# Kernel tuning notes

Hardware: AMD Instinct MI355X
Metric: run time of the kernel (lower is better)

Reference implementation:

```python
import jax, jax.numpy as jnp
import numpy as np

N = 50000      # nodes
E = 800000     # directed edges (avg degree 16)
IN, HID, OUT = 256, 128, 16


def setup_inputs() -> dict:
    key = jax.random.key(0)
    ks = jax.random.split(key, 8)
    x = jax.random.normal(ks[0], (N, IN), dtype=jnp.float32)
    edge_index = jax.random.randint(ks[1], (2, E), 0, N)
    W1 = jax.random.normal(ks[2], (IN, HID), dtype=jnp.float32) * (1.0 / np.sqrt(IN))
    b1 = jnp.zeros((HID,), jnp.float32)
    W2 = jax.random.normal(ks[3], (HID, HID), dtype=jnp.float32) * (1.0 / np.sqrt(HID))
    b2 = jnp.zeros((HID,), jnp.float32)
    Wc = jax.random.normal(ks[4], (HID, OUT), dtype=jnp.float32) * (1.0 / np.sqrt(HID))
    bc = jnp.zeros((OUT,), jnp.float32)
    return {"x": x, "W1": W1, "b1": b1, "W2": W2, "b2": b2,
            "Wc": Wc, "bc": bc, "edge_index": edge_index, "conv_time": 30}


def _gcn_norm(edge_index, n, dtype):
    # add self-loops, compute symmetric GCN normalization D^{-1/2}(A+I)D^{-1/2}
    loops = jnp.arange(n)
    src = jnp.concatenate([edge_index[0], loops])
    dst = jnp.concatenate([edge_index[1], loops])
    deg = jax.ops.segment_sum(jnp.ones_like(dst, dtype=dtype), dst, num_segments=n)
    dinv = jnp.where(deg > 0, jax.lax.rsqrt(deg), jnp.zeros_like(deg))
    norm = dinv[src] * dinv[dst]          # [E+N] edge weights
    return src, dst, norm


def _propagate(h, src, dst, norm, n, hops):
    # hops is a static Python int (conv_time)
    for _ in range(hops):
        h = jax.ops.segment_sum(h[src] * norm[:, None], dst, num_segments=n)
    return h


def reference(x, W1, b1, W2, b2, Wc, bc, edge_index, conv_time):
    n = x.shape[0]
    src, dst, norm = _gcn_norm(edge_index, n, x.dtype)
    # conv1: linear only (conv_time = 0)
    h = jax.nn.relu(x @ W1 + b1)
    # dropout is identity in eval mode
    # conv2: linear + conv_time hops of normalized propagation
    h = _propagate(h @ W2 + b2, src, dst, norm, n, int(conv_time))
    h = jax.nn.relu(h)
    # cls: linear + 1 hop
    h = _propagate(h @ Wc + bc, src, dst, norm, n, 1)
    return h
```

## Files before the change

kernel.cpp:

```cpp
#include <hip/hip_runtime.h>
#include <hip/hip_fp16.h>

#define NNODES 50000
#define NEDGES 800000
#define IN_F   256
#define HID_F  128
#define OUT_F  16
#define HOPS   30
#define MPAD   50048

typedef unsigned int u32;
typedef unsigned long long u64;
typedef _Float16 f16;
typedef f16 f16x8 __attribute__((ext_vector_type(8)));
typedef float f32x4 __attribute__((ext_vector_type(4)));
typedef u32 u32x4 __attribute__((ext_vector_type(4)));

union U32H2 { u32 u; __half2 h; };

__device__ inline float2 upk(u32 v) {
    U32H2 t; t.u = v;
    return __half22float2(t.h);
}
__device__ inline u32 pk2(float a, float b) {
    U32H2 t; t.h = __floats2half2_rn(a, b);
    return t.u;
}


__global__ void k_init_deg(int* __restrict__ deg, int n) {
    int i = blockIdx.x * blockDim.x + threadIdx.x;
    if (i < n) deg[i] = 1;
}

__global__ void k_count(const int* __restrict__ dst, int* __restrict__ deg, int e) {
    int i = blockIdx.x * blockDim.x + threadIdx.x;
    if (i < e) atomicAdd(&deg[dst[i]], 1);
}

__global__ void k_dinv(const int* __restrict__ deg, float* __restrict__ dinv, int n) {
    int i = blockIdx.x * blockDim.x + threadIdx.x;
    if (i < n) dinv[i] = rsqrtf((float)deg[i]);
}

__global__ void k_scan1(const int* __restrict__ deg, int* __restrict__ bsums, int n) {
    __shared__ int sh[256];
    int tid = threadIdx.x;
    int i = blockIdx.x * 256 + tid;
    sh[tid] = (i < n) ? deg[i] : 0;
    __syncthreads();
    for (int ofs = 128; ofs > 0; ofs >>= 1) {
        if (tid < ofs) sh[tid] += sh[tid + ofs];
        __syncthreads();
    }
    if (tid == 0) bsums[blockIdx.x] = sh[0];
}

__global__ void k_scan2(int* __restrict__ bsums, int nb, int* __restrict__ rp, int n) {
    if (threadIdx.x == 0 && blockIdx.x == 0) {
        int run = 0;
        for (int b = 0; b < nb; ++b) { int t = bsums[b]; bsums[b] = run; run += t; }
        rp[n] = run;
    }
}

__global__ void k_scan3(const int* __restrict__ deg, const int* __restrict__ bsums,
                        int* __restrict__ rp, int* __restrict__ cursor, int n) {
    __shared__ int sh[256];
    int tid = threadIdx.x;
    int i = blockIdx.x * 256 + tid;
    int v = (i < n) ? deg[i] : 0;
    sh[tid] = v;
    __syncthreads();
    for (int ofs = 1; ofs < 256; ofs <<= 1) {
        int t = 0;
        if (tid >= ofs) t = sh[tid - ofs];
        __syncthreads();
        sh[tid] += t;
        __syncthreads();
    }
    if (i < n) {
        int excl = sh[tid] - v + bsums[blockIdx.x];
        rp[i] = excl;
        cursor[i] = excl;
    }
}

__global__ void k_scatter(const int* __restrict__ src, const int* __restrict__ dst,
                          const float* __restrict__ dinv, int* __restrict__ cursor,
                          int2* __restrict__ ew, int e, int n) {
    int t = blockIdx.x * blockDim.x + threadIdx.x;
    if (t < e) {
        int s = src[t], d = dst[t];
        int pos = atomicAdd(&cursor[d], 1);
        ew[pos] = make_int2(s, __float_as_int(dinv[s] * dinv[d]));
    } else if (t < e + n) {
        int i = t - e;
        int pos = atomicAdd(&cursor[i], 1);
        float di = dinv[i];
        ew[pos] = make_int2(i, __float_as_int(di * di));
    }
}

__global__ void k_sortwave(const int* __restrict__ rp, int2* __restrict__ ew, int n) {
    int node = blockIdx.x * 4 + (threadIdx.x >> 6);
    int lane = threadIdx.x & 63;
    if (node >= n) return;
    int beg = rp[node], end = rp[node + 1];
    int deg = end - beg;
    if (deg > 64) return;
    int2 my = make_int2(0x7fffffff, 0);
    if (lane < deg) my = ew[beg + lane];
    int rank = 0;
    for (int k = 0; k < deg; ++k) {
        int sk = __shfl(my.x, k);
        rank += (sk < my.x) || (sk == my.x && k < lane);
    }
    if (lane < deg) ew[beg + rank] = my;
}

template<int K, int NC>
__global__ void k_cast_wt(const float* __restrict__ W, f16* __restrict__ Wt) {
    int i = blockIdx.x * blockDim.x + threadIdx.x;
    if (i < K * NC) {
        int k = i / NC, c = i % NC;
        Wt[(size_t)c * K + k] = (f16)W[i];
    }
}


template<int K, bool RELU, typename TA>
__global__ __launch_bounds__(256)
void k_gemm_mfma(const TA* __restrict__ A, const f16* __restrict__ Wt,
                 const float* __restrict__ b, f16* __restrict__ C, int M) {
    __shared__ f16 sa[64][K + 8];
    int tid  = threadIdx.x;
    int wid  = tid >> 6;
    int lane = tid & 63;
    int row0 = blockIdx.x * 64;
    int rowW = row0 + wid * 16;
    int rl   = lane & 15;
    int kc   = (lane >> 4) * 8;

    if constexpr (sizeof(TA) == 4) {
        const float4* A4 = reinterpret_cast<const float4*>(A);
        constexpr int C4 = K / 4;
        for (int idx = tid; idx < 64 * C4; idx += 256) {
            int r  = idx / C4;
            int c4 = idx % C4;
            int gr = row0 + r;
            if (gr >= M) gr = M - 1;
            float4 v = A4[(size_t)gr * C4 + c4];
            f16 o[4] = {(f16)v.x, (f16)v.y, (f16)v.z, (f16)v.w};
            *reinterpret_cast<u64*>(&sa[r][c4 * 4]) = *reinterpret_cast<u64*>(o);
        }
    } else {
        const u32x4* A4 = reinterpret_cast<const u32x4*>(A);
        constexpr int C8 = K / 8;
        for (int idx = tid; idx < 64 * C8; idx += 256) {
            int r  = idx / C8;
            int c8 = idx % C8;
            int gr = row0 + r;
            if (gr >= M) gr = M - 1;
            u32x4 v = A4[(size_t)gr * C8 + c8];
            *reinterpret_cast<u32x4*>(&sa[r][c8 * 8]) = v;
        }
    }
    __syncthreads();

    f32x4 acc[8];
#pragma unroll
    for (int n = 0; n < 8; ++n) acc[n] = (f32x4)0.f;

    int lr = wid * 16 + rl;
#pragma unroll
    for (int k0 = 0; k0 < K; k0 += 32) {
        f16x8 aF = *reinterpret_cast<const f16x8*>(&sa[lr][k0 + kc]);
#pragma unroll
        for (int n = 0; n < 8; ++n) {
            f16x8 bF = *reinterpret_cast<const f16x8*>(
                Wt + (size_t)(n * 16 + rl) * K + k0 + kc);
            acc[n] = __builtin_amdgcn_mfma_f32_16x16x32_f16(aF, bF, acc[n], 0, 0, 0);
        }
    }

#pragma unroll
    for (int n = 0; n < 8; ++n) {
        int col = n * 16 + rl;
        float bias = b[col];
#pragma unroll
        for (int j = 0; j < 4; ++j) {
            int row = rowW + 4 * (lane >> 4) + j;
            if (row < M) {
                float s = acc[n][j] + bias;
                if (RELU) s = fmaxf(s, 0.f);
                C[(size_t)row * 128 + col] = (f16)s;
            }
        }
    }
}


template<bool RELU>
__global__ void k_proph(const u32* __restrict__ Hin, u32* __restrict__ Hout,
                        const int* __restrict__ rp, const int2* __restrict__ ew,
                        int n) {
    int grp  = threadIdx.x >> 4;
    int lane = threadIdx.x & 15;
    int node = blockIdx.x * 16 + grp;
    if (node >= n) return;
    int beg = rp[node], end = rp[node + 1];
    const u32x4* H4 = reinterpret_cast<const u32x4*>(Hin);

    float acc[8];
#pragma unroll
    for (int i = 0; i < 8; ++i) acc[i] = 0.f;

    auto body = [&](int e) {
        int2 p   = ew[e];
        float ww = __int_as_float(p.y);
        u32x4 v  = H4[(size_t)p.x * 16 + lane];
#pragma unroll
        for (int q = 0; q < 4; ++q) {
            float2 f = upk(v[q]);
            acc[q * 2 + 0] += ww * f.x;
            acc[q * 2 + 1] += ww * f.y;
        }
    };

    int e = beg;
    for (; e + 1 < end; e += 2) { body(e); body(e + 1); }
    if (e < end) body(e);

    if (RELU) {
#pragma unroll
        for (int i = 0; i < 8; ++i) acc[i] = fmaxf(acc[i], 0.f);
    }
    u32x4 o;
#pragma unroll
    for (int q = 0; q < 4; ++q) o[q] = pk2(acc[q * 2], acc[q * 2 + 1]);
    reinterpret_cast<u32x4*>(Hout)[(size_t)node * 16 + lane] = o;
}


__global__ void k_cls_h(const u32* __restrict__ Ah, const float* __restrict__ Wc,
                        const float* __restrict__ bc, float* __restrict__ G, int M) {
    __shared__ float sa[64][132];
    __shared__ float4 sw4[512];
    int tid  = threadIdx.x;
    int row0 = blockIdx.x * 64;

    for (int idx = tid; idx < 512; idx += 256)
        sw4[idx] = reinterpret_cast<const float4*>(Wc)[idx];

    const uint4* A4 = reinterpret_cast<const uint4*>(Ah);
    for (int idx = tid; idx < 64 * 16; idx += 256) {
        int r = idx >> 4, c = idx & 15;
        int gr = row0 + r;
        uint4 v = (gr < M) ? A4[(size_t)gr * 16 + c]
                           : make_uint4(0u, 0u, 0u, 0u);
        float* dst = &sa[r][c * 8];
        const u32* vv = reinterpret_cast<const u32*>(&v);
#pragma unroll
        for (int q = 0; q < 4; ++q) {
            float2 f = upk(vv[q]);
            dst[q * 2 + 0] = f.x;
            dst[q * 2 + 1] = f.y;
        }
    }
    __syncthreads();

    int tc = tid & 3;
    int tr = tid >> 2;
    float4 acc = make_float4(0.f, 0.f, 0.f, 0.f);
    for (int k4 = 0; k4 < 32; ++k4) {
        float4 a = *reinterpret_cast<const float4*>(&sa[tr][k4 * 4]);
        const float* af = reinterpret_cast<const float*>(&a);
#pragma unroll
        for (int kk = 0; kk < 4; ++kk) {
            float4 wv = sw4[(k4 * 4 + kk) * 4 + tc];
            float av = af[kk];
            acc.x += av * wv.x; acc.y += av * wv.y;
            acc.z += av * wv.z; acc.w += av * wv.w;
        }
    }
    int r = row0 + tr;
    if (r < M) {
        float4 bb = reinterpret_cast<const float4*>(bc)[tc];
        acc.x += bb.x; acc.y += bb.y; acc.z += bb.z; acc.w += bb.w;
        reinterpret_cast<float4*>(G)[(size_t)r * 4 + tc] = acc;
    }
}


__global__ void k_prop16(const float* __restrict__ Gin, float* __restrict__ Out,
                         const int* __restrict__ rp, const int2* __restrict__ ew,
                         int n) {
    int g    = blockIdx.x * 64 + (threadIdx.x >> 2);
    int lane = threadIdx.x & 3;
    if (g >= n) return;
    int beg = rp[g], end = rp[g + 1];
    const float4* G4 = reinterpret_cast<const float4*>(Gin);
    float ax = 0.f, ay = 0.f, az = 0.f, aw = 0.f;
    for (int e = beg; e < end; ++e) {
        int2 p   = ew[e];
        float ww = __int_as_float(p.y);
        float4 hv = G4[(size_t)p.x * 4 + lane];
        ax += ww * hv.x; ay += ww * hv.y; az += ww * hv.z; aw += ww * hv.w;
    }
    reinterpret_cast<float4*>(Out)[(size_t)g * 4 + lane] = make_float4(ax, ay, az, aw);
}


extern "C" void kernel_launch(void* const* d_in, const int* in_sizes, int n_in,
                              void* d_out, int out_size, void* d_ws, size_t ws_size,
                              hipStream_t stream) {
    const float* x  = (const float*)d_in[0];
    const float* W1 = (const float*)d_in[1];
    const float* b1 = (const float*)d_in[2];
    const float* W2 = (const float*)d_in[3];
    const float* b2 = (const float*)d_in[4];
    const float* Wc = (const float*)d_in[5];
    const float* bc = (const float*)d_in[6];
    const int*   ei = (const int*)d_in[7];
    const int* srcp = ei;
    const int* dstp = ei + NEDGES;
    float* out = (float*)d_out;

    char* p = (char*)d_ws;
    auto alloc = [&](size_t bytes) -> char* {
        char* r = p;
        p += (bytes + 255) & ~(size_t)255;
        return r;
    };
    int*   deg    = (int*)  alloc(NNODES * 4);
    float* dinv   = (float*)alloc(NNODES * 4);
    int*   rp     = (int*)  alloc((NNODES + 1) * 4);
    int*   cursor = (int*)  alloc(NNODES * 4);
    int*   bsums  = (int*)  alloc(256 * 4);
    int2*  ew     = (int2*) alloc((size_t)(NEDGES + NNODES) * 8);
    f16*   W1t    = (f16*)  alloc((size_t)HID_F * IN_F * 2);
    f16*   W2t    = (f16*)  alloc((size_t)HID_F * HID_F * 2);
    f16*   H0h    = (f16*)  alloc((size_t)MPAD * HID_F * 2);
    u32*   Hh0    = (u32*)  alloc((size_t)MPAD * HID_F * 2);
    u32*   Hh1    = (u32*)  alloc((size_t)NNODES * HID_F * 2);
    float* G      = (float*)alloc((size_t)NNODES * OUT_F * 4);

    const int T = 256;
    auto nb = [](int n, int t) { return (n + t - 1) / t; };

    k_init_deg<<<nb(NNODES, T), T, 0, stream>>>(deg, NNODES);
    k_count<<<nb(NEDGES, T), T, 0, stream>>>(dstp, deg, NEDGES);
    k_dinv<<<nb(NNODES, T), T, 0, stream>>>(deg, dinv, NNODES);
    int NB = nb(NNODES, 256);
    k_scan1<<<NB, 256, 0, stream>>>(deg, bsums, NNODES);
    k_scan2<<<1, 1, 0, stream>>>(bsums, NB, rp, NNODES);
    k_scan3<<<NB, 256, 0, stream>>>(deg, bsums, rp, cursor, NNODES);
    k_scatter<<<nb(NEDGES + NNODES, T), T, 0, stream>>>(srcp, dstp, dinv, cursor,
                                                        ew, NEDGES, NNODES);
    k_sortwave<<<nb(NNODES, 4), 256, 0, stream>>>(rp, ew, NNODES);

    k_cast_wt<IN_F,  HID_F><<<nb(IN_F * HID_F, T), T, 0, stream>>>(W1, W1t);
    k_cast_wt<HID_F, HID_F><<<nb(HID_F * HID_F, T), T, 0, stream>>>(W2, W2t);

    int GB = MPAD / 64;
    k_gemm_mfma<IN_F,  true,  float><<<GB, 256, 0, stream>>>(x,   W1t, b1, H0h, NNODES);
    k_gemm_mfma<HID_F, false, f16  ><<<GB, 256, 0, stream>>>(H0h, W2t, b2, (f16*)Hh0, NNODES);

    u32* cur = Hh0;
    u32* nxt = Hh1;
    int PB = nb(NNODES, 16);
    for (int i = 0; i < HOPS; ++i) {
        if (i == HOPS - 1)
            k_proph<true ><<<PB, 256, 0, stream>>>(cur, nxt, rp, ew, NNODES);
        else
            k_proph<false><<<PB, 256, 0, stream>>>(cur, nxt, rp, ew, NNODES);
        u32* t = cur; cur = nxt; nxt = t;
    }

    k_cls_h<<<nb(NNODES, 64), 256, 0, stream>>>(cur, Wc, bc, G, NNODES);
    k_prop16<<<nb(NNODES, 64), 256, 0, stream>>>(G, out, rp, ew, NNODES);
}
```

Before: 1.094 ms.

## Bucket nodes by degree for propagation and stage GEMM weights in LDS

Builds a degree histogram and counting-sort permutation so the 30 propagation hops process nodes grouped by similar degree. This is meant to reduce load imbalance between the 16-lane groups within a wavefront. Separately, the MFMA GEMM now loads weight tiles into shared memory in K-chunks instead of reading B fragments directly from global memory. The costs are an extra indirection per node, output writes and rp reads that are no longer coalesced, and more LDS use in the GEMM.

```diff
diff --git a/kernel.cpp b/kernel.cpp
--- a/kernel.cpp
+++ b/kernel.cpp
@@ -119,6 +119,28 @@
     if (lane < deg) ew[beg + rank] = my;
 }
 
+
+__global__ void k_hist(const int* __restrict__ deg, int* __restrict__ hist, int n) {
+    int i = blockIdx.x * blockDim.x + threadIdx.x;
+    if (i < n) atomicAdd(&hist[min(deg[i], 64)], 1);
+}
+
+__global__ void k_histscan(int* __restrict__ hist, int* __restrict__ bincur) {
+    if (threadIdx.x == 0 && blockIdx.x == 0) {
+        int run = 0;
+        for (int b = 0; b <= 64; ++b) { int t = hist[b]; bincur[b] = run; run += t; }
+    }
+}
+
+__global__ void k_permscatter(const int* __restrict__ deg, int* __restrict__ bincur,
+                              int* __restrict__ perm, int n) {
+    int i = blockIdx.x * blockDim.x + threadIdx.x;
+    if (i < n) {
+        int pos = atomicAdd(&bincur[min(deg[i], 64)], 1);
+        perm[pos] = i;
+    }
+}
+
 template<int K, int NC>
 __global__ void k_cast_wt(const float* __restrict__ W, f16* __restrict__ Wt) {
     int i = blockIdx.x * blockDim.x + threadIdx.x;
@@ -133,7 +155,9 @@
 __global__ __launch_bounds__(256)
 void k_gemm_mfma(const TA* __restrict__ A, const f16* __restrict__ Wt,
                  const float* __restrict__ b, f16* __restrict__ C, int M) {
-    __shared__ f16 sa[64][K + 8];
+    constexpr int KC = (K > 128) ? 128 : K;
+    __shared__ f16 sa[64][KC + 8];
+    __shared__ f16 sb[128][KC + 8];
     int tid  = threadIdx.x;
     int wid  = tid >> 6;
     int lane = tid & 63;
@@ -142,45 +166,59 @@
     int rl   = lane & 15;
     int kc   = (lane >> 4) * 8;
 
-    if constexpr (sizeof(TA) == 4) {
-        const float4* A4 = reinterpret_cast<const float4*>(A);
-        constexpr int C4 = K / 4;
-        for (int idx = tid; idx < 64 * C4; idx += 256) {
-            int r  = idx / C4;
-            int c4 = idx % C4;
-            int gr = row0 + r;
-            if (gr >= M) gr = M - 1;
-            float4 v = A4[(size_t)gr * C4 + c4];
-            f16 o[4] = {(f16)v.x, (f16)v.y, (f16)v.z, (f16)v.w};
-            *reinterpret_cast<u64*>(&sa[r][c4 * 4]) = *reinterpret_cast<u64*>(o);
-        }
-    } else {
-        const u32x4* A4 = reinterpret_cast<const u32x4*>(A);
-        constexpr int C8 = K / 8;
-        for (int idx = tid; idx < 64 * C8; idx += 256) {
-            int r  = idx / C8;
-            int c8 = idx % C8;
-            int gr = row0 + r;
-            if (gr >= M) gr = M - 1;
-            u32x4 v = A4[(size_t)gr * C8 + c8];
-            *reinterpret_cast<u32x4*>(&sa[r][c8 * 8]) = v;
-        }
-    }
-    __syncthreads();
-
     f32x4 acc[8];
 #pragma unroll
     for (int n = 0; n < 8; ++n) acc[n] = (f32x4)0.f;
 
     int lr = wid * 16 + rl;
-#pragma unroll
-    for (int k0 = 0; k0 < K; k0 += 32) {
-        f16x8 aF = *reinterpret_cast<const f16x8*>(&sa[lr][k0 + kc]);
-#pragma unroll
-        for (int n = 0; n < 8; ++n) {
-            f16x8 bF = *reinterpret_cast<const f16x8*>(
-                Wt + (size_t)(n * 16 + rl) * K + k0 + kc);
-            acc[n] = __builtin_amdgcn_mfma_f32_16x16x32_f16(aF, bF, acc[n], 0, 0, 0);
+
+    for (int c = 0; c < K / KC; ++c) {
+        int k0 = c * KC;
+        if (c > 0) __syncthreads();
+        if constexpr (sizeof(TA) == 4) {
+            const float4* A4 = reinterpret_cast<const float4*>(A);
+            constexpr int C4 = KC / 4;
+            for (int idx = tid; idx < 64 * C4; idx += 256) {
+                int r  = idx / C4;
+                int c4 = idx % C4;
+                int gr = row0 + r;
+                if (gr >= M) gr = M - 1;
+                float4 v = A4[(size_t)gr * (K / 4) + k0 / 4 + c4];
+                f16 o[4] = {(f16)v.x, (f16)v.y, (f16)v.z, (f16)v.w};
+                *reinterpret_cast<u64*>(&sa[r][c4 * 4]) = *reinterpret_cast<u64*>(o);
+            }
+        } else {
+            const u32x4* A4 = reinterpret_cast<const u32x4*>(A);
+            constexpr int C8 = KC / 8;
+            for (int idx = tid; idx < 64 * C8; idx += 256) {
+                int r  = idx / C8;
+                int c8 = idx % C8;
+                int gr = row0 + r;
+                if (gr >= M) gr = M - 1;
+                u32x4 v = A4[(size_t)gr * (K / 8) + k0 / 8 + c8];
+                *reinterpret_cast<u32x4*>(&sa[r][c8 * 8]) = v;
+            }
+        }
+        {
+            const u32x4* B4 = reinterpret_cast<const u32x4*>(Wt);
+            constexpr int C8 = KC / 8;
+            for (int idx = tid; idx < 128 * C8; idx += 256) {
+                int r  = idx / C8;
+                int c8 = idx % C8;
+                u32x4 v = B4[(size_t)r * (K / 8) + k0 / 8 + c8];
+                *reinterpret_cast<u32x4*>(&sb[r][c8 * 8]) = v;
+            }
+        }
+        __syncthreads();
+
+#pragma unroll
+        for (int kk = 0; kk < KC; kk += 32) {
+            f16x8 aF = *reinterpret_cast<const f16x8*>(&sa[lr][kk + kc]);
+#pragma unroll
+            for (int n = 0; n < 8; ++n) {
+                f16x8 bF = *reinterpret_cast<const f16x8*>(&sb[n * 16 + rl][kk + kc]);
+                acc[n] = __builtin_amdgcn_mfma_f32_16x16x32_f16(aF, bF, acc[n], 0, 0, 0);
+            }
         }
     }
 
@@ -204,11 +242,12 @@
 template<bool RELU>
 __global__ void k_proph(const u32* __restrict__ Hin, u32* __restrict__ Hout,
                         const int* __restrict__ rp, const int2* __restrict__ ew,
-                        int n) {
+                        const int* __restrict__ perm, int n) {
     int grp  = threadIdx.x >> 4;
     int lane = threadIdx.x & 15;
-    int node = blockIdx.x * 16 + grp;
-    if (node >= n) return;
+    int g    = blockIdx.x * 16 + grp;
+    if (g >= n) return;
+    int node = perm[g];
     int beg = rp[node], end = rp[node + 1];
     const u32x4* H4 = reinterpret_cast<const u32x4*>(Hin);
 
@@ -338,6 +377,9 @@
     int*   rp     = (int*)  alloc((NNODES + 1) * 4);
     int*   cursor = (int*)  alloc(NNODES * 4);
     int*   bsums  = (int*)  alloc(256 * 4);
+    int*   hist   = (int*)  alloc(65 * 4);
+    int*   bincur = (int*)  alloc(65 * 4);
+    int*   perm   = (int*)  alloc(NNODES * 4);
     int2*  ew     = (int2*) alloc((size_t)(NEDGES + NNODES) * 8);
     f16*   W1t    = (f16*)  alloc((size_t)HID_F * IN_F * 2);
     f16*   W2t    = (f16*)  alloc((size_t)HID_F * HID_F * 2);
@@ -359,6 +401,10 @@
     k_scatter<<<nb(NEDGES + NNODES, T), T, 0, stream>>>(srcp, dstp, dinv, cursor,
                                                         ew, NEDGES, NNODES);
     k_sortwave<<<nb(NNODES, 4), 256, 0, stream>>>(rp, ew, NNODES);
+    hipMemsetAsync(hist, 0, 65 * 4, stream);
+    k_hist<<<nb(NNODES, T), T, 0, stream>>>(deg, hist, NNODES);
+    k_histscan<<<1, 1, 0, stream>>>(hist, bincur);
+    k_permscatter<<<nb(NNODES, T), T, 0, stream>>>(deg, bincur, perm, NNODES);
 
     k_cast_wt<IN_F,  HID_F><<<nb(IN_F * HID_F, T), T, 0, stream>>>(W1, W1t);
     k_cast_wt<HID_F, HID_F><<<nb(HID_F * HID_F, T), T, 0, stream>>>(W2, W2t);
@@ -372,9 +418,9 @@
     int PB = nb(NNODES, 16);
     for (int i = 0; i < HOPS; ++i) {
         if (i == HOPS - 1)
-            k_proph<true ><<<PB, 256, 0, stream>>>(cur, nxt, rp, ew, NNODES);
+            k_proph<true ><<<PB, 256, 0, stream>>>(cur, nxt, rp, ew, perm, NNODES);
         else
-            k_proph<false><<<PB, 256, 0, stream>>>(cur, nxt, rp, ew, NNODES);
+            k_proph<false><<<PB, 256, 0, stream>>>(cur, nxt, rp, ew, perm, NNODES);
         u32* t = cur; cur = nxt; nxt = t;
     }
 
```

New measurement: 1.401 ms. +28.0%, slower.
